# Performance work log

Hardware: AMD Instinct MI355X
Metric: run time of the kernel (lower is better)

## Reference

```python
import jax, jax.numpy as jnp
import numpy as np

K = 16

def _local_cov(points):
    # points: [B, N, 3]. FoldingNet-style local covariance feature.
    xx = jnp.sum(points * points, axis=-1)                       # [B,N]
    inner = jnp.einsum('bnd,bmd->bnm', points, points)           # [B,N,N]
    pd = -xx[:, :, None] + 2.0 * inner - xx[:, None, :]          # negative sq dist
    _, idx = jax.lax.top_k(pd, K)                                # [B,N,K] nearest first (self at 0)
    n0 = jnp.take_along_axis(points, idx[:, :, 0][:, :, None], axis=1)  # [B,N,3]
    n1 = jnp.take_along_axis(points, idx[:, :, 1][:, :, None], axis=1)  # [B,N,3]
    cov = n0[..., :, None] * n1[..., None, :]                    # [B,N,3,3] outer product
    B, N = points.shape[0], points.shape[1]
    return jnp.concatenate([points, cov.reshape(B, N, 9)], axis=-1)     # [B,N,12]

def _stage(x, w1, b1, wr, br, w2, b2):
    h = jax.nn.relu(x @ w1 + b1)
    h = jax.nn.relu(h + (h @ wr + br))   # ResidualLinearLayer then ReLU
    return h @ w2 + b2                   # [B,N,1]

def setup_inputs() -> dict:
    key = jax.random.key(0)
    ks = jax.random.split(key, 16)
    B, N, F = 8, 4096, 512
    s = 0.02
    d = {
        'latent': jax.random.normal(ks[0], (B, N, F), jnp.float32),
        'reconstructed_points': jax.random.normal(ks[1], (B, 3, N), jnp.float32),
        's1_w1': jax.random.normal(ks[2], (F + 12, F), jnp.float32) * s,
        's1_b1': jnp.zeros((F,), jnp.float32),
        's1_wr': jax.random.normal(ks[3], (F, F), jnp.float32) * s,
        's1_br': jnp.zeros((F,), jnp.float32),
        's1_w2': jax.random.normal(ks[4], (F, 1), jnp.float32) * s,
        's1_b2': jnp.zeros((1,), jnp.float32),
        's2_w1': jax.random.normal(ks[5], (F + 1, F), jnp.float32) * s,
        's2_b1': jnp.zeros((F,), jnp.float32),
        's2_wr': jax.random.normal(ks[6], (F, F), jnp.float32) * s,
        's2_br': jnp.zeros((F,), jnp.float32),
        's2_w2': jax.random.normal(ks[7], (F, 1), jnp.float32) * s,
        's2_b2': jnp.zeros((1,), jnp.float32),
        's3_w1': jax.random.normal(ks[8], (F + 1, F), jnp.float32) * s,
        's3_b1': jnp.zeros((F,), jnp.float32),
        's3_wr': jax.random.normal(ks[9], (F, F), jnp.float32) * s,
        's3_br': jnp.zeros((F,), jnp.float32),
        's3_w2': jax.random.normal(ks[10], (F, 1), jnp.float32) * s,
        's3_b2': jnp.zeros((1,), jnp.float32),
    }
    return d

def reference(latent, reconstructed_points,
              s1_w1, s1_b1, s1_wr, s1_br, s1_w2, s1_b2,
              s2_w1, s2_b1, s2_wr, s2_br, s2_w2, s2_b2,
              s3_w1, s3_b1, s3_wr, s3_br, s3_w2, s3_b2):
    pts = jnp.transpose(reconstructed_points, (0, 2, 1))   # [B,N,3]
    local = _local_cov(pts)                                 # [B,N,12]
    f1 = jnp.concatenate([latent, local], axis=-1)
    std1 = _stage(f1, s1_w1, s1_b1, s1_wr, s1_br, s1_w2, s1_b2)
    f2 = jnp.concatenate([latent, std1], axis=-1)
    std2 = std1 + _stage(f2, s2_w1, s2_b1, s2_wr, s2_br, s2_w2, s2_b2)
    f3 = jnp.concatenate([latent, std2], axis=-1)
    std3 = std2 + _stage(f3, s3_w1, s3_b1, s3_wr, s3_br, s3_w2, s3_b2)
    return std3   # [B,N,1]
```

## Files before the change

kernel.cpp:

```cpp
#include <hip/hip_runtime.h>

typedef __bf16 bf16x8 __attribute__((ext_vector_type(8)));
typedef float f32x16 __attribute__((ext_vector_type(16)));

__device__ __forceinline__ unsigned short f2bf(float f) {
  unsigned u = __float_as_uint(f);
  u += 0x7FFFu + ((u >> 16) & 1u);
  return (unsigned short)(u >> 16);
}

__device__ __forceinline__ void gload_lds16(const void* g, void* l) {
  __builtin_amdgcn_global_load_lds((const __attribute__((address_space(1))) void*)g,
                                   (__attribute__((address_space(3))) void*)l,
                                   16, 0, 0);
}

#define NPTS 4096
#define LDX 576

__global__ __launch_bounds__(256) void convw6_kernel(
    const float* w0, const float* w1, const float* w2,
    const float* r0, const float* r1, const float* r2,
    unsigned short* d0, unsigned short* d1, unsigned short* d2,
    unsigned short* e0, unsigned short* e1, unsigned short* e2) {
  int z = blockIdx.z;
  const float* src; unsigned short* dst; int Ksrc, Kpad, addI;
  switch (z) {
    case 0: src = w0; dst = d0; Ksrc = 524; Kpad = 576; addI = 0; break;
    case 1: src = w1; dst = d1; Ksrc = 513; Kpad = 576; addI = 0; break;
    case 2: src = w2; dst = d2; Ksrc = 513; Kpad = 576; addI = 0; break;
    case 3: src = r0; dst = e0; Ksrc = 512; Kpad = 512; addI = 1; break;
    case 4: src = r1; dst = e1; Ksrc = 512; Kpad = 512; addI = 1; break;
    default: src = r2; dst = e2; Ksrc = 512; Kpad = 512; addI = 1; break;
  }
  int k0 = blockIdx.x * 32;
  if (k0 >= Kpad) return;
  __shared__ float tile[32][33];
  int n0 = blockIdx.y * 32;
  int tx = threadIdx.x & 31, ty = threadIdx.x >> 5;
#pragma unroll
  for (int r = 0; r < 32; r += 8) {
    int k = k0 + ty + r, n = n0 + tx;
    tile[ty + r][tx] = (k < Ksrc) ? src[(size_t)k * 512 + n] : 0.f;
  }
  __syncthreads();
#pragma unroll
  for (int r = 0; r < 32; r += 8) {
    int n = n0 + ty + r, k = k0 + tx;
    float v = tile[tx][ty + r];
    if (addI && n == k) v += 1.0f;
    dst[(size_t)n * Kpad + k] = f2bf(v);
  }
}

__global__ __launch_bounds__(256) void conv_latent_kernel(const float* __restrict__ latent,
                                                          unsigned short* __restrict__ X) {
  size_t idx = (size_t)blockIdx.x * 256 + threadIdx.x;
  size_t m = idx >> 7;
  int c4 = (int)(idx & 127) * 4;
  float4 v = *(const float4*)(latent + m * 512 + c4);
  ushort4 o;
  o.x = f2bf(v.x); o.y = f2bf(v.y); o.z = f2bf(v.z); o.w = f2bf(v.w);
  *(ushort4*)(X + m * LDX + c4) = o;
}

__device__ __forceinline__ void merge1(float& v, int& j, int mk) {
  float ov = __shfl_xor(v, mk); int oj = __shfl_xor(j, mk);
  bool take = (ov > v) || (ov == v && oj < j);
  v = take ? ov : v; j = take ? oj : j;
}

__global__ __launch_bounds__(512) void knn_kernel(const float* __restrict__ rp,
                                                  unsigned short* __restrict__ X) {
  __shared__ float4 P[NPTS];
  int b = blockIdx.y;
  const float* base = rp + (size_t)b * 3 * NPTS;
  for (int j = threadIdx.x; j < NPTS; j += 512) {
    float x = base[j], y = base[NPTS + j], z = base[2 * NPTS + j];
    float xx = __fadd_rn(__fadd_rn(__fmul_rn(x, x), __fmul_rn(y, y)), __fmul_rn(z, z));
    P[j] = make_float4(x, y, z, -xx);
  }
  __syncthreads();
  int wave = threadIdx.x >> 6, lane = threadIdx.x & 63;
  int grp = lane >> 4, slice = lane & 15;
  int il0 = wave * 8 + grp * 2;
  int ia = blockIdx.x * 64 + il0;
  int ib = ia + 1;
  float4 pa = P[ia], pb = P[ib];
  float ax = 2.f * pa.x, ay = 2.f * pa.y, az = 2.f * pa.z;
  float bx = 2.f * pb.x, by = 2.f * pb.y, bz = 2.f * pb.z;
  float va = -3.4e38f, vb = -3.4e38f;
  int ta = 0, tb = 0;
  int sta = ((ia & 15) == slice) ? (ia >> 4) : -1;
  int stb = ((ib & 15) == slice) ? (ib >> 4) : -1;
  const float4* pp = P + slice;
#pragma unroll 8
  for (int t = 0; t < NPTS / 16; ++t) {
    float4 pj = pp[t * 16];
    float ea = __builtin_fmaf(ax, pj.x, __builtin_fmaf(ay, pj.y,
               __builtin_fmaf(az, pj.z, pj.w)));
    float eb = __builtin_fmaf(bx, pj.x, __builtin_fmaf(by, pj.y,
               __builtin_fmaf(bz, pj.z, pj.w)));
    ea = (t == sta) ? -3.4e38f : ea;
    eb = (t == stb) ? -3.4e38f : eb;
    bool ca = ea > va; va = ca ? ea : va; ta = ca ? t : ta;
    bool cb = eb > vb; vb = cb ? eb : vb; tb = cb ? t : tb;
  }
  int ja = ta * 16 + slice, jb = tb * 16 + slice;
#pragma unroll
  for (int mk = 1; mk <= 8; mk <<= 1) {
    merge1(va, ja, mk);
    merge1(vb, jb, mk);
  }
  if (slice == 0) {
#pragma unroll
    for (int p = 0; p < 2; ++p) {
      float4 pi = (p == 0) ? pa : pb;
      float4 p1 = P[(p == 0) ? ja : jb];
      size_t row = (size_t)b * NPTS + ia + p;
      unsigned short* xp = X + row * LDX + 512;
      float vals[12] = { pi.x, pi.y, pi.z,
                         pi.x * p1.x, pi.x * p1.y, pi.x * p1.z,
                         pi.y * p1.x, pi.y * p1.y, pi.y * p1.z,
                         pi.z * p1.x, pi.z * p1.y, pi.z * p1.z };
#pragma unroll
      for (int k = 0; k < 12; ++k) xp[k] = f2bf(vals[k]);
#pragma unroll
      for (int k = 12; k < 32; ++k) xp[k] = 0;
    }
  }
}

#define BM 128
#define BN 128
#define BK 64
#define GRP 520
#define MBLK 256

__global__ __launch_bounds__(256) void gemm_relu_kernel(
    const unsigned short* __restrict__ Xb, const unsigned short* __restrict__ Wt,
    const float* __restrict__ bias, unsigned short* __restrict__ H,
    int K, int ldx, int ldw,
    const float* __restrict__ stdv, const float* __restrict__ w1row) {
  __shared__ unsigned short As[16 * GRP];
  __shared__ unsigned short Bs[16 * GRP];
  const int t = threadIdx.x;
  const int wave = t >> 6, lane = t & 63;
  const int flat = blockIdx.x;
  const int m0 = (flat & (MBLK - 1)) * BM;
  const int n0 = (flat >> 8) * BN;
  const int wm = (wave >> 1) * 64, wn = (wave & 1) * 64;
  const int srow = lane >> 3;
  const int sslot = (lane & 7) ^ srow;
  const int l31 = lane & 31, hi = lane >> 5;
  const int w7 = l31 & 7, g2 = l31 >> 3;
  const unsigned short* Arow = Xb + (size_t)(m0 + srow) * ldx + sslot * 8;
  const unsigned short* Brow = Wt + (size_t)(n0 + srow) * ldw + sslot * 8;
  f32x16 acc[2][2] = {};
  for (int kt = 0; kt < K; kt += BK) {
#pragma unroll
    for (int r = 0; r < 4; ++r) {
      int g = wave + r * 4;
      gload_lds16(Arow + (size_t)g * 8 * ldx + kt, As + g * GRP);
      gload_lds16(Brow + (size_t)g * 8 * ldw + kt, Bs + g * GRP);
    }
    __syncthreads();
#pragma unroll
    for (int ks = 0; ks < 4; ++ks) {
      int qx = (ks * 2 + hi) ^ w7;
      bf16x8 a[2], bb[2];
#pragma unroll
      for (int i = 0; i < 2; ++i)
        a[i] = *(const bf16x8*)(As + ((wm >> 3) + i * 4 + g2) * GRP + w7 * 64 + qx * 8);
#pragma unroll
      for (int j = 0; j < 2; ++j)
        bb[j] = *(const bf16x8*)(Bs + ((wn >> 3) + j * 4 + g2) * GRP + w7 * 64 + qx * 8);
#pragma unroll
      for (int i = 0; i < 2; ++i)
#pragma unroll
        for (int j = 0; j < 2; ++j)
          acc[i][j] = __builtin_amdgcn_mfma_f32_32x32x16_bf16(a[i], bb[j], acc[i][j], 0, 0, 0);
    }
    __syncthreads();
  }
  if (w1row) {
    float wv[2];
#pragma unroll
    for (int j = 0; j < 2; ++j) wv[j] = w1row[n0 + wn + j * 32 + l31];
#pragma unroll
    for (int i = 0; i < 2; ++i) {
#pragma unroll
      for (int rg = 0; rg < 16; ++rg) {
        int row = m0 + wm + i * 32 + (rg & 3) + 8 * (rg >> 2) + 4 * hi;
        float sv = stdv[row];
#pragma unroll
        for (int j = 0; j < 2; ++j) acc[i][j][rg] += sv * wv[j];
      }
    }
  }
#pragma unroll
  for (int j = 0; j < 2; ++j) {
    int col = n0 + wn + j * 32 + l31;
    float bv = bias[col];
#pragma unroll
    for (int i = 0; i < 2; ++i) {
#pragma unroll
      for (int rg = 0; rg < 16; ++rg) {
        int row = m0 + wm + i * 32 + (rg & 3) + 8 * (rg >> 2) + 4 * hi;
        float v = acc[i][j][rg] + bv;
        v = v > 0.f ? v : 0.f;
        H[(size_t)row * 512 + col] = f2bf(v);
      }
    }
  }
}

__global__ __launch_bounds__(256) void gemm_res_kernel(
    const unsigned short* __restrict__ H1, const unsigned short* __restrict__ Wt,
    const float* __restrict__ br, const float* __restrict__ w2,
    float* __restrict__ so) {
  __shared__ unsigned short As[16 * GRP];
  __shared__ unsigned short Bs[16 * GRP];
  const int t = threadIdx.x;
  const int wave = t >> 6, lane = t & 63;
  const int flat = blockIdx.x;
  const int m0 = (flat & (MBLK - 1)) * BM;
  const int n0 = (flat >> 8) * BN;
  const int wm = (wave >> 1) * 64, wn = (wave & 1) * 64;
  const int srow = lane >> 3;
  const int sslot = (lane & 7) ^ srow;
  const int l31 = lane & 31, hi = lane >> 5;
  const int w7 = l31 & 7, g2 = l31 >> 3;
  const unsigned short* Arow = H1 + (size_t)(m0 + srow) * 512 + sslot * 8;
  const unsigned short* Brow = Wt + (size_t)(n0 + srow) * 512 + sslot * 8;
  f32x16 acc[2][2] = {};
  for (int kt = 0; kt < 512; kt += BK) {
#pragma unroll
    for (int r = 0; r < 4; ++r) {
      int g = wave + r * 4;
      gload_lds16(Arow + (size_t)g * 8 * 512 + kt, As + g * GRP);
      gload_lds16(Brow + (size_t)g * 8 * 512 + kt, Bs + g * GRP);
    }
    __syncthreads();
#pragma unroll
    for (int ks = 0; ks < 4; ++ks) {
      int qx = (ks * 2 + hi) ^ w7;
      bf16x8 a[2], bb[2];
#pragma unroll
      for (int i = 0; i < 2; ++i)
        a[i] = *(const bf16x8*)(As + ((wm >> 3) + i * 4 + g2) * GRP + w7 * 64 + qx * 8);
#pragma unroll
      for (int j = 0; j < 2; ++j)
        bb[j] = *(const bf16x8*)(Bs + ((wn >> 3) + j * 4 + g2) * GRP + w7 * 64 + qx * 8);
#pragma unroll
      for (int i = 0; i < 2; ++i)
#pragma unroll
        for (int j = 0; j < 2; ++j)
          acc[i][j] = __builtin_amdgcn_mfma_f32_32x32x16_bf16(a[i], bb[j], acc[i][j], 0, 0, 0);
    }
    __syncthreads();
  }
  float bv[2], wv[2];
#pragma unroll
  for (int j = 0; j < 2; ++j) {
    int col = n0 + wn + j * 32 + l31;
    bv[j] = br[col]; wv[j] = w2[col];
  }
#pragma unroll
  for (int i = 0; i < 2; ++i) {
#pragma unroll
    for (int rg = 0; rg < 16; ++rg) {
      float s = 0.f;
#pragma unroll
      for (int j = 0; j < 2; ++j) {
        float v = acc[i][j][rg] + bv[j];
        v = v > 0.f ? v : 0.f;
        s += v * wv[j];
      }
      s += __shfl_xor(s, 1); s += __shfl_xor(s, 2); s += __shfl_xor(s, 4);
      s += __shfl_xor(s, 8); s += __shfl_xor(s, 16);
      if (l31 == 0) {
        int row = m0 + wm + i * 32 + (rg & 3) + 8 * (rg >> 2) + 4 * hi;
        atomicAdd(&so[row], s);
      }
    }
  }
}

__global__ __launch_bounds__(256) void init_so_kernel(float* so, const float* b2) {
  int m = blockIdx.x * 256 + threadIdx.x;
  so[m] = b2[0];
}
__global__ __launch_bounds__(256) void update_kernel(float* std_cum, float* so,
                                                     const float* b2_next, int first) {
  int m = blockIdx.x * 256 + threadIdx.x;
  float s = so[m];
  if (!first) s += std_cum[m];
  std_cum[m] = s;
  so[m] = b2_next[0];
}
__global__ __launch_bounds__(256) void finalize_kernel(float* out, const float* std_cum,
                                                       const float* so) {
  int m = blockIdx.x * 256 + threadIdx.x;
  out[m] = std_cum[m] + so[m];
}

extern "C" void kernel_launch(void* const* d_in, const int* in_sizes, int n_in,
                              void* d_out, int out_size, void* d_ws, size_t ws_size,
                              hipStream_t stream) {
  const int B = 8, N = NPTS, M = B * N;
  const float* latent = (const float*)d_in[0];
  const float* rp = (const float*)d_in[1];
  const float* w1[3] = {(const float*)d_in[2], (const float*)d_in[8], (const float*)d_in[14]};
  const float* b1[3] = {(const float*)d_in[3], (const float*)d_in[9], (const float*)d_in[15]};
  const float* wr[3] = {(const float*)d_in[4], (const float*)d_in[10], (const float*)d_in[16]};
  const float* br[3] = {(const float*)d_in[5], (const float*)d_in[11], (const float*)d_in[17]};
  const float* w2[3] = {(const float*)d_in[6], (const float*)d_in[12], (const float*)d_in[18]};
  const float* b2[3] = {(const float*)d_in[7], (const float*)d_in[13], (const float*)d_in[19]};

  char* ws = (char*)d_ws;
  auto carve = [&](size_t bytes) {
    char* p = ws;
    ws += (bytes + 255) & ~(size_t)255;
    return p;
  };
  unsigned short* X  = (unsigned short*)carve((size_t)M * LDX * 2);
  unsigned short* H1 = (unsigned short*)carve((size_t)M * 512 * 2);
  unsigned short* W1t[3], *Wrt[3];
  for (int s = 0; s < 3; ++s) W1t[s] = (unsigned short*)carve((size_t)512 * LDX * 2);
  for (int s = 0; s < 3; ++s) Wrt[s] = (unsigned short*)carve((size_t)512 * 512 * 2);
  float* std_cum = (float*)carve((size_t)M * 4);
  float* so      = (float*)carve((size_t)M * 4);

  convw6_kernel<<<dim3(LDX / 32, 16, 6), 256, 0, stream>>>(
      w1[0], w1[1], w1[2], wr[0], wr[1], wr[2],
      W1t[0], W1t[1], W1t[2], Wrt[0], Wrt[1], Wrt[2]);
  conv_latent_kernel<<<(M * 128) / 256, 256, 0, stream>>>(latent, X);
  knn_kernel<<<dim3(N / 64, B), 512, 0, stream>>>(rp, X);
  init_so_kernel<<<M / 256, 256, 0, stream>>>(so, b2[0]);

  for (int s = 0; s < 3; ++s) {
    if (s == 0) {
      gemm_relu_kernel<<<dim3((M / BM) * (512 / BN)), 256, 0, stream>>>(
          X, W1t[s], b1[s], H1, LDX, LDX, LDX, nullptr, nullptr);
    } else {
      gemm_relu_kernel<<<dim3((M / BM) * (512 / BN)), 256, 0, stream>>>(
          X, W1t[s], b1[s], H1, 512, LDX, LDX, std_cum, w1[s] + (size_t)512 * 512);
    }
    gemm_res_kernel<<<dim3((M / BM) * (512 / BN)), 256, 0, stream>>>(
        H1, Wrt[s], br[s], w2[s], so);
    if (s < 2)
      update_kernel<<<M / 256, 256, 0, stream>>>(std_cum, so, b2[s + 1], s == 0 ? 1 : 0);
  }
  finalize_kernel<<<M / 256, 256, 0, stream>>>((float*)d_out, std_cum, so);
}
```

Measured before the change: 373.6 us.

## Double-buffer GEMM LDS tiles and drop per-stage update kernels

Both GEMM kernels now use double-buffered dynamic LDS, so the next K-tile's global-to-LDS loads are issued before the current tile is computed. A partial vmcnt wait and raw s_barrier replace the paired __syncthreads, aiming to hide load latency behind the MFMA work. Each stage also gets its own output accumulator, initialised once, with the residual sum formed inside the GEMM epilogue and the finalize kernel. This removes the two update kernel launches. The cost is doubled LDS use (about 66 KB per block), which may lower occupancy, plus hand-written waitcnt counts that must match the number of outstanding loads.

```diff
diff --git a/kernel.cpp b/kernel.cpp
--- a/kernel.cpp
+++ b/kernel.cpp
@@ -136,14 +136,15 @@
 #define BK 64
 #define GRP 520
 #define MBLK 256
+#define BUFU16 (32 * GRP)
 
 __global__ __launch_bounds__(256) void gemm_relu_kernel(
     const unsigned short* __restrict__ Xb, const unsigned short* __restrict__ Wt,
     const float* __restrict__ bias, unsigned short* __restrict__ H,
     int K, int ldx, int ldw,
-    const float* __restrict__ stdv, const float* __restrict__ w1row) {
-  __shared__ unsigned short As[16 * GRP];
-  __shared__ unsigned short Bs[16 * GRP];
+    const float* __restrict__ std1, const float* __restrict__ std2,
+    const float* __restrict__ w1row) {
+  extern __shared__ unsigned short S[];
   const int t = threadIdx.x;
   const int wave = t >> 6, lane = t & 63;
   const int flat = blockIdx.x;
@@ -157,31 +158,45 @@
   const unsigned short* Arow = Xb + (size_t)(m0 + srow) * ldx + sslot * 8;
   const unsigned short* Brow = Wt + (size_t)(n0 + srow) * ldw + sslot * 8;
   f32x16 acc[2][2] = {};
-  for (int kt = 0; kt < K; kt += BK) {
+  const int nt = K / BK;
+  auto STAGE = [&](int buf, int kt) {
 #pragma unroll
     for (int r = 0; r < 4; ++r) {
       int g = wave + r * 4;
-      gload_lds16(Arow + (size_t)g * 8 * ldx + kt, As + g * GRP);
-      gload_lds16(Brow + (size_t)g * 8 * ldw + kt, Bs + g * GRP);
-    }
-    __syncthreads();
+      gload_lds16(Arow + (size_t)g * 8 * ldx + kt, S + buf * BUFU16 + g * GRP);
+      gload_lds16(Brow + (size_t)g * 8 * ldw + kt, S + buf * BUFU16 + (16 + g) * GRP);
+    }
+  };
+  STAGE(0, 0);
+  for (int tt = 0; tt < nt; ++tt) {
+    const int cur = tt & 1;
+    if (tt + 1 < nt) {
+      STAGE(cur ^ 1, (tt + 1) * BK);
+      asm volatile("s_waitcnt vmcnt(8)" ::: "memory");
+    } else {
+      asm volatile("s_waitcnt vmcnt(0)" ::: "memory");
+    }
+    __builtin_amdgcn_s_barrier();
+    const unsigned short* Sa = S + cur * BUFU16;
+    const unsigned short* Sb = Sa + 16 * GRP;
 #pragma unroll
     for (int ks = 0; ks < 4; ++ks) {
       int qx = (ks * 2 + hi) ^ w7;
       bf16x8 a[2], bb[2];
 #pragma unroll
       for (int i = 0; i < 2; ++i)
-        a[i] = *(const bf16x8*)(As + ((wm >> 3) + i * 4 + g2) * GRP + w7 * 64 + qx * 8);
+        a[i] = *(const bf16x8*)(Sa + ((wm >> 3) + i * 4 + g2) * GRP + w7 * 64 + qx * 8);
 #pragma unroll
       for (int j = 0; j < 2; ++j)
-        bb[j] = *(const bf16x8*)(Bs + ((wn >> 3) + j * 4 + g2) * GRP + w7 * 64 + qx * 8);
+        bb[j] = *(const bf16x8*)(Sb + ((wn >> 3) + j * 4 + g2) * GRP + w7 * 64 + qx * 8);
 #pragma unroll
       for (int i = 0; i < 2; ++i)
 #pragma unroll
         for (int j = 0; j < 2; ++j)
           acc[i][j] = __builtin_amdgcn_mfma_f32_32x32x16_bf16(a[i], bb[j], acc[i][j], 0, 0, 0);
     }
-    __syncthreads();
+    __builtin_amdgcn_sched_barrier(0);
+    __builtin_amdgcn_s_barrier();
   }
   if (w1row) {
     float wv[2];
@@ -192,7 +207,8 @@
 #pragma unroll
       for (int rg = 0; rg < 16; ++rg) {
         int row = m0 + wm + i * 32 + (rg & 3) + 8 * (rg >> 2) + 4 * hi;
-        float sv = stdv[row];
+        float sv = std1[row];
+        if (std2) sv += std2[row];
 #pragma unroll
         for (int j = 0; j < 2; ++j) acc[i][j][rg] += sv * wv[j];
       }
@@ -219,8 +235,7 @@
     const unsigned short* __restrict__ H1, const unsigned short* __restrict__ Wt,
     const float* __restrict__ br, const float* __restrict__ w2,
     float* __restrict__ so) {
-  __shared__ unsigned short As[16 * GRP];
-  __shared__ unsigned short Bs[16 * GRP];
+  extern __shared__ unsigned short S[];
   const int t = threadIdx.x;
   const int wave = t >> 6, lane = t & 63;
   const int flat = blockIdx.x;
@@ -234,31 +249,45 @@
   const unsigned short* Arow = H1 + (size_t)(m0 + srow) * 512 + sslot * 8;
   const unsigned short* Brow = Wt + (size_t)(n0 + srow) * 512 + sslot * 8;
   f32x16 acc[2][2] = {};
-  for (int kt = 0; kt < 512; kt += BK) {
+  auto STAGE = [&](int buf, int kt) {
 #pragma unroll
     for (int r = 0; r < 4; ++r) {
       int g = wave + r * 4;
-      gload_lds16(Arow + (size_t)g * 8 * 512 + kt, As + g * GRP);
-      gload_lds16(Brow + (size_t)g * 8 * 512 + kt, Bs + g * GRP);
-    }
-    __syncthreads();
+      gload_lds16(Arow + (size_t)g * 8 * 512 + kt, S + buf * BUFU16 + g * GRP);
+      gload_lds16(Brow + (size_t)g * 8 * 512 + kt, S + buf * BUFU16 + (16 + g) * GRP);
+    }
+  };
+  STAGE(0, 0);
+  const int nt = 512 / BK;
+  for (int tt = 0; tt < nt; ++tt) {
+    const int cur = tt & 1;
+    if (tt + 1 < nt) {
+      STAGE(cur ^ 1, (tt + 1) * BK);
+      asm volatile("s_waitcnt vmcnt(8)" ::: "memory");
+    } else {
+      asm volatile("s_waitcnt vmcnt(0)" ::: "memory");
+    }
+    __builtin_amdgcn_s_barrier();
+    const unsigned short* Sa = S + cur * BUFU16;
+    const unsigned short* Sb = Sa + 16 * GRP;
 #pragma unroll
     for (int ks = 0; ks < 4; ++ks) {
       int qx = (ks * 2 + hi) ^ w7;
       bf16x8 a[2], bb[2];
 #pragma unroll
       for (int i = 0; i < 2; ++i)
-        a[i] = *(const bf16x8*)(As + ((wm >> 3) + i * 4 + g2) * GRP + w7 * 64 + qx * 8);
+        a[i] = *(const bf16x8*)(Sa + ((wm >> 3) + i * 4 + g2) * GRP + w7 * 64 + qx * 8);
 #pragma unroll
       for (int j = 0; j < 2; ++j)
-        bb[j] = *(const bf16x8*)(Bs + ((wn >> 3) + j * 4 + g2) * GRP + w7 * 64 + qx * 8);
+        bb[j] = *(const bf16x8*)(Sb + ((wn >> 3) + j * 4 + g2) * GRP + w7 * 64 + qx * 8);
 #pragma unroll
       for (int i = 0; i < 2; ++i)
 #pragma unroll
         for (int j = 0; j < 2; ++j)
           acc[i][j] = __builtin_amdgcn_mfma_f32_32x32x16_bf16(a[i], bb[j], acc[i][j], 0, 0, 0);
     }
-    __syncthreads();
+    __builtin_amdgcn_sched_barrier(0);
+    __builtin_amdgcn_s_barrier();
   }
   float bv[2], wv[2];
 #pragma unroll
@@ -287,22 +316,18 @@
   }
 }
 
-__global__ __launch_bounds__(256) void init_so_kernel(float* so, const float* b2) {
+__global__ __launch_bounds__(256) void init_so3_kernel(float* so0, float* so1, float* so2,
+                                                       const float* b2_0, const float* b2_1,
+                                                       const float* b2_2) {
   int m = blockIdx.x * 256 + threadIdx.x;
-  so[m] = b2[0];
-}
-__global__ __launch_bounds__(256) void update_kernel(float* std_cum, float* so,
-                                                     const float* b2_next, int first) {
+  so0[m] = b2_0[0];
+  so1[m] = b2_1[0];
+  so2[m] = b2_2[0];
+}
+__global__ __launch_bounds__(256) void finalize_kernel(float* out, const float* so0,
+                                                       const float* so1, const float* so2) {
   int m = blockIdx.x * 256 + threadIdx.x;
-  float s = so[m];
-  if (!first) s += std_cum[m];
-  std_cum[m] = s;
-  so[m] = b2_next[0];
-}
-__global__ __launch_bounds__(256) void finalize_kernel(float* out, const float* std_cum,
-                                                       const float* so) {
-  int m = blockIdx.x * 256 + threadIdx.x;
-  out[m] = std_cum[m] + so[m];
+  out[m] = so0[m] + so1[m] + so2[m];
 }
 
 extern "C" void kernel_launch(void* const* d_in, const int* in_sizes, int n_in,
@@ -329,28 +354,31 @@
   unsigned short* W1t[3], *Wrt[3];
   for (int s = 0; s < 3; ++s) W1t[s] = (unsigned short*)carve((size_t)512 * LDX * 2);
   for (int s = 0; s < 3; ++s) Wrt[s] = (unsigned short*)carve((size_t)512 * 512 * 2);
-  float* std_cum = (float*)carve((size_t)M * 4);
-  float* so      = (float*)carve((size_t)M * 4);
+  float* so0 = (float*)carve((size_t)M * 4);
+  float* so1 = (float*)carve((size_t)M * 4);
+  float* so2 = (float*)carve((size_t)M * 4);
+
+  const size_t ldsBytes = (size_t)2 * BUFU16 * 2;
 
   convw6_kernel<<<dim3(LDX / 32, 16, 6), 256, 0, stream>>>(
       w1[0], w1[1], w1[2], wr[0], wr[1], wr[2],
       W1t[0], W1t[1], W1t[2], Wrt[0], Wrt[1], Wrt[2]);
   conv_latent_kernel<<<(M * 128) / 256, 256, 0, stream>>>(latent, X);
   knn_kernel<<<dim3(N / 64, B), 512, 0, stream>>>(rp, X);
-  init_so_kernel<<<M / 256, 256, 0, stream>>>(so, b2[0]);
-
+  init_so3_kernel<<<M / 256, 256, 0, stream>>>(so0, so1, so2, b2[0], b2[1], b2[2]);
+
+  float* soArr[3] = {so0, so1, so2};
   for (int s = 0; s < 3; ++s) {
     if (s == 0) {
-      gemm_relu_kernel<<<dim3((M / BM) * (512 / BN)), 256, 0, stream>>>(
-          X, W1t[s], b1[s], H1, LDX, LDX, LDX, nullptr, nullptr);
+      gemm_relu_kernel<<<dim3((M / BM) * (512 / BN)), 256, ldsBytes, stream>>>(
+          X, W1t[s], b1[s], H1, LDX, LDX, LDX, nullptr, nullptr, nullptr);
     } else {
-      gemm_relu_kernel<<<dim3((M / BM) * (512 / BN)), 256, 0, stream>>>(
-          X, W1t[s], b1[s], H1, 512, LDX, LDX, std_cum, w1[s] + (size_t)512 * 512);
-    }
-    gemm_res_kernel<<<dim3((M / BM) * (512 / BN)), 256, 0, stream>>>(
-        H1, Wrt[s], br[s], w2[s], so);
-    if (s < 2)
-      update_kernel<<<M / 256, 256, 0, stream>>>(std_cum, so, b2[s + 1], s == 0 ? 1 : 0);
-  }
-  finalize_kernel<<<M / 256, 256, 0, stream>>>((float*)d_out, std_cum, so);
-}
+      gemm_relu_kernel<<<dim3((M / BM) * (512 / BN)), 256, ldsBytes, stream>>>(
+          X, W1t[s], b1[s], H1, 512, LDX, LDX,
+          so0, (s == 2) ? so1 : nullptr, w1[s] + (size_t)512 * 512);
+    }
+    gemm_res_kernel<<<dim3((M / BM) * (512 / BN)), 256, ldsBytes, stream>>>(
+        H1, Wrt[s], br[s], w2[s], soArr[s]);
+  }
+  finalize_kernel<<<M / 256, 256, 0, stream>>>((float*)d_out, so0, so1, so2);
+}
```

New measurement: 368.0 us. Within noise of the previous version (-1.5%).
